# Kernel optimization log

Measured on AMD Instinct MI355X. Metric: run time of the kernel, lower is better.

The kernel has to match this reference:

```python
import jax, jax.numpy as jnp
import numpy as np

N = 51200      # num nodes
E = 614400     # num edges
G = 256        # num graphs
T = 8          # num target capsules (GCNConv heads)
D = 128        # in_channels == out_channels
ROUTES = 3     # num_routes
BN_EPS = 1e-5


def squash(s):
    # s: (..., D). v = |s|^2/(1+|s|^2) * s/|s|
    s2 = jnp.sum(s * s, axis=-1, keepdims=True)
    return (s2 / (1.0 + s2)) * s * jax.lax.rsqrt(s2 + 1e-16)


def setup_inputs() -> dict:
    key = jax.random.key(0)
    k0, k1, k2, k3 = jax.random.split(key, 4)
    x = jax.random.normal(k0, (N, D), dtype=jnp.float32)
    edge_index = jax.random.randint(k1, (2, E), 0, N, dtype=jnp.int32)
    batch = jnp.sort(jax.random.randint(k2, (N,), 0, G, dtype=jnp.int32))
    edge_weight = jnp.ones((E,), dtype=jnp.float32)
    gamma = jnp.ones((D,), dtype=jnp.float32)
    beta = jnp.zeros((D,), dtype=jnp.float32)
    W = jax.random.normal(k3, (T, D, D), dtype=jnp.float32) * (1.0 / np.sqrt(D))
    bias = jnp.zeros((T, D), dtype=jnp.float32)
    return {"x": x, "edge_weight": edge_weight, "gamma": gamma, "beta": beta,
            "W": W, "bias": bias, "edge_index": edge_index, "batch": batch}


def reference(x, edge_weight, gamma, beta, W, bias, edge_index, batch):
    n = x.shape[0]
    row, col = edge_index[0], edge_index[1]

    # BatchNorm1d (training-mode batch stats)
    mu = jnp.mean(x, axis=0)
    var = jnp.var(x, axis=0)
    x = (x - mu) * jax.lax.rsqrt(var + BN_EPS) * gamma + beta

    # --- GCNConv per target capsule (PyG gcn_norm with self-loops) ---
    sl = jnp.arange(n, dtype=row.dtype)
    row_sl = jnp.concatenate([row, sl])
    col_sl = jnp.concatenate([col, sl])
    w_sl = jnp.concatenate([edge_weight, jnp.ones((n,), x.dtype)])
    deg = jax.ops.segment_sum(w_sl, col_sl, num_segments=n)
    dis = jnp.where(deg > 0, jax.lax.rsqrt(jnp.maximum(deg, 1e-12)), 0.0)
    norm = dis[row_sl] * w_sl * dis[col_sl]          # (E+N,)

    xW = jnp.einsum('nd,tdo->nto', x, W)             # (N, T, D)
    caps = []
    for t in range(T):  # small fixed loop over capsule heads keeps edge msgs at (E+N, D)
        msg = norm[:, None] * xW[row_sl, t]          # (E+N, D)
        caps.append(jax.ops.segment_sum(msg, col_sl, num_segments=n) + bias[t])
    u_hat = jnp.stack(caps, axis=1)                  # (N, T, D)

    # --- dynamic routing ---
    node_deg = jax.ops.segment_sum(edge_weight, row, num_segments=n)  # original edges, no self loops
    b = jnp.broadcast_to(node_deg[:, None, None], (n, T, 1))
    u_det = jax.lax.stop_gradient(u_hat)
    for _ in range(ROUTES - 1):
        c = jax.nn.softmax(b, axis=1)                               # (N, T, 1)
        s = jax.ops.segment_sum(c * u_det, batch, num_segments=G)   # (G, T, D)
        v = squash(s)[batch]                                        # (N, T, D)
        b = b + jnp.sum(u_det * v, axis=-1, keepdims=True)

    c = jax.nn.softmax(b, axis=1)
    s = jax.ops.segment_sum(c * u_hat, batch, num_segments=G)        # (G, T, D)
    cnt = jax.ops.segment_sum(jnp.ones((n,), x.dtype), batch, num_segments=G)
    x_mean = jax.ops.segment_sum(x, batch, num_segments=G) / jnp.maximum(cnt, 1.0)[:, None]
    s = s + x_mean[:, None, :]
    v = squash(s)
    # final_layer=True: per-capsule L2 norm -> (G, T)
    return jnp.sqrt(jnp.sum(v * v, axis=-1) + 1e-16)
```

## Files before the change

### kernel.cpp

```cpp
#include <hip/hip_runtime.h>
#include <hip/hip_bf16.h>
#include <math.h>

#define N_NODES 51200
#define N_EDGES 614400
#define N_GRAPHS 256
#define T_CAPS 8
#define D_DIM 128
#define BN_EPS 1e-5f
#define RCAP 256
#define NBUCK 200
#define BCAP 4096
#define EPB 4096
#define SBLK 150
typedef __attribute__((ext_vector_type(8))) __bf16 bf16x8;
typedef __attribute__((ext_vector_type(8))) unsigned short ushort8;
typedef __attribute__((ext_vector_type(4))) float f32x4;

__device__ inline f32x4 mfma16(uint4 a, uint4 b, f32x4 c) {
  return __builtin_amdgcn_mfma_f32_16x16x32_bf16(
      __builtin_bit_cast(bf16x8, a), __builtin_bit_cast(bf16x8, b), c, 0, 0, 0);
}
__device__ inline f32x4 mfma16v(uint4 a, ushort8 b, f32x4 c) {
  return __builtin_amdgcn_mfma_f32_16x16x32_bf16(
      __builtin_bit_cast(bf16x8, a), __builtin_bit_cast(bf16x8, b), c, 0, 0, 0);
}

__device__ inline float waveReduceSum(float v) {
#pragma unroll
  for (int off = 1; off < 64; off <<= 1) v += __shfl_xor(v, off, 64);
  return v;
}
__device__ inline float bf_lo(unsigned u) { return __uint_as_float(u << 16); }
__device__ inline float bf_hi(unsigned u) { return __uint_as_float(u & 0xffff0000u); }
__device__ inline unsigned bfbits(float f) {
  unsigned u = __float_as_uint(f);
  return (u + 0x7FFFu + ((u >> 16) & 1u)) >> 16;
}

__global__ void __launch_bounds__(256) prep(const int* __restrict__ batch,
                                            const float* __restrict__ W,
                                            int* __restrict__ start, int* __restrict__ bcur,
                                            unsigned* __restrict__ Wfrag,
                                            unsigned* __restrict__ WTfrag,
                                            float* __restrict__ rawzero) {
  int i = blockIdx.x * 256 + threadIdx.x;
  if (i < NBUCK) bcur[i] = 0;
  for (int j = i; j < 2 * N_GRAPHS * D_DIM; j += N_NODES) rawzero[j] = 0.f;
  int bn = batch[i];
  if (i == 0) {
    for (int g = 0; g <= bn; g++) start[g] = 0;
  } else {
    int bp = batch[i - 1];
    for (int g = bp + 1; g <= bn; g++) start[g] = i;
  }
  if (i == N_NODES - 1)
    for (int g = bn + 1; g <= N_GRAPHS; g++) start[g] = N_NODES;
  for (int dd = i; dd < 65536; dd += N_NODES) {
    int jj = dd & 3, lane = (dd >> 2) & 63, ks = (dd >> 8) & 3;
    int nt = (dd >> 10) & 7, t = dd >> 13;
    int k = ks * 32 + ((lane >> 4) << 3) + 2 * jj;
    int n = nt * 16 + (lane & 15);
    float a = W[(t << 14) + (k << 7) + n];
    float b = W[(t << 14) + ((k + 1) << 7) + n];
    Wfrag[dd] = bfbits(a) | (bfbits(b) << 16);
    float2 w2 = ((const float2*)W)[((t << 14) + (n << 7) + k) >> 1];
    WTfrag[dd] = bfbits(w2.x) | (bfbits(w2.y) << 16);
  }
}

__global__ void __launch_bounds__(512) scatter_x(
    const int* __restrict__ row, const int* __restrict__ col, const float* __restrict__ ew,
    int* __restrict__ bcur, uint2* __restrict__ ebuck, const float* __restrict__ x,
    const int* __restrict__ start, float* __restrict__ rawxsum, float* __restrict__ rawxsq) {
  int bid = blockIdx.x, tid = threadIdx.x;
  __shared__ uint2 staged[EPB];
  __shared__ int hcnt[256], lbase[256], gbase[256], wpart[8];
  if (bid < SBLK) {
    unsigned rx[8], ry[8];
    int bk[8], idx[8];
    int e4 = bid * 1024 + tid;
#pragma unroll
    for (int h = 0; h < 2; h++) {
      int4 c4 = ((const int4*)col)[e4 + h * 512];
      int4 r4 = ((const int4*)row)[e4 + h * 512];
      float4 w4 = ((const float4*)ew)[e4 + h * 512];
      int o = h * 4;
      rx[o] = ((unsigned)c4.x << 16) | (unsigned)r4.x; ry[o] = bfbits(w4.x); bk[o] = c4.x >> 8;
      rx[o+1] = ((unsigned)c4.y << 16) | (unsigned)r4.y; ry[o+1] = bfbits(w4.y); bk[o+1] = c4.y >> 8;
      rx[o+2] = ((unsigned)c4.z << 16) | (unsigned)r4.z; ry[o+2] = bfbits(w4.z); bk[o+2] = c4.z >> 8;
      rx[o+3] = ((unsigned)c4.w << 16) | (unsigned)r4.w; ry[o+3] = bfbits(w4.w); bk[o+3] = c4.w >> 8;
    }
    if (tid < 256) hcnt[tid] = 0;
    __syncthreads();
#pragma unroll
    for (int k = 0; k < 8; k++) idx[k] = atomicAdd(&hcnt[bk[k]], 1);
    __syncthreads();
    int v = (tid < 256) ? hcnt[tid] : 0;
    int lane = tid & 63, wid = tid >> 6;
    int s = v;
#pragma unroll
    for (int off = 1; off < 64; off <<= 1) {
      int t = __shfl_up(s, off, 64);
      if (lane >= off) s += t;
    }
    if (lane == 63) wpart[wid] = s;
    if (tid < NBUCK) gbase[tid] = atomicAdd(&bcur[tid], v);
    __syncthreads();
    int add = 0;
    for (int w2 = 0; w2 < wid; w2++) add += wpart[w2];
    if (tid < 256) lbase[tid] = s + add - v;
    __syncthreads();
#pragma unroll
    for (int k = 0; k < 8; k++) staged[lbase[bk[k]] + idx[k]] = make_uint2(rx[k], ry[k]);
    __syncthreads();
    for (int i = tid; i < EPB; i += 512) {
      uint2 r = staged[i];
      int b = r.x >> 24;
      int pos = gbase[b] + (i - lbase[b]);
      if (pos < BCAP) ebuck[b * BCAP + pos] = r;
    }
    return;
  }
  int b2 = bid - SBLK;
  int g = b2 >> 2, sub = b2 & 3;
  float* ls = (float*)staged;
  float* ls2 = ls + 16 * 128;
  int q = tid & 31, h = tid >> 5;
  int st = start[g], en = start[g + 1];
  const float4* x4 = (const float4*)x;
  float4 s = make_float4(0.f, 0.f, 0.f, 0.f), s2 = make_float4(0.f, 0.f, 0.f, 0.f);
  for (int n = st + sub * 16 + h; n < en; n += 64) {
    float4 v = x4[n * 32 + q];
    s.x += v.x; s.y += v.y; s.z += v.z; s.w += v.w;
    s2.x += v.x * v.x; s2.y += v.y * v.y; s2.z += v.z * v.z; s2.w += v.w * v.w;
  }
  *(float4*)&ls[h * 128 + 4 * q] = s;
  *(float4*)&ls2[h * 128 + 4 * q] = s2;
  __syncthreads();
  if (tid < 128) {
    float a = 0.f;
#pragma unroll
    for (int hh = 0; hh < 16; hh++) a += ls[hh * 128 + tid];
    atomicAdd(&rawxsum[g * D_DIM + tid], a);
  } else if (tid < 256) {
    int d = tid - 128;
    float a = 0.f;
#pragma unroll
    for (int hh = 0; hh < 16; hh++) a += ls2[hh * 128 + d];
    atomicAdd(&rawxsq[g * D_DIM + d], a);
  }
}

__global__ void __launch_bounds__(512) mid(const float* __restrict__ rawxsum,
                                           const float* __restrict__ rawxsq,
                                           const float* __restrict__ gamma,
                                           const float* __restrict__ beta,
                                           float* __restrict__ scale,
                                           float* __restrict__ shift,
                                           const uint2* __restrict__ ebuck,
                                           const int* __restrict__ bcur,
                                           unsigned* __restrict__ csr,
                                           int* __restrict__ nstart, int* __restrict__ ncnt,
                                           float* __restrict__ dis) {
  int bid = blockIdx.x, tid = threadIdx.x;
  __shared__ uint2 staged[BCAP];
  __shared__ unsigned outr[BCAP];
  __shared__ int hist[256], pref[256], cur[256], wpart[8];
  if (bid < 128) {
    int d = bid;
    float* ls = (float*)staged;
    float* ls2 = ls + 256;
    if (tid < 256) {
      ls[tid] = rawxsum[tid * D_DIM + d];
      ls2[tid] = rawxsq[tid * D_DIM + d];
    }
    __syncthreads();
    for (int off = 128; off; off >>= 1) {
      if (tid < off) {
        ls[tid] += ls[tid + off];
        ls2[tid] += ls2[tid + off];
      }
      __syncthreads();
    }
    if (tid == 0) {
      float mu = ls[0] * (1.0f / N_NODES);
      float var = ls2[0] * (1.0f / N_NODES) - mu * mu;
      float rstd = rsqrtf(var + BN_EPS);
      float sc = gamma[d] * rstd;
      scale[d] = sc;
      shift[d] = beta[d] - mu * sc;
    }
    return;
  }
  int b = bid - 128;
  int cnt = min(bcur[b], BCAP);
  for (int i = tid; i < cnt; i += 512) staged[i] = ebuck[b * BCAP + i];
  if (tid < 256) hist[tid] = 0;
  __syncthreads();
  for (int i = tid; i < cnt; i += 512) {
    int dl = (staged[i].x >> 16) & 255;
    atomicAdd(&hist[dl], 1);
  }
  __syncthreads();
  int v = (tid < 256) ? hist[tid] : 0;
  int lane = tid & 63, wid = tid >> 6;
  int s = v;
#pragma unroll
  for (int off = 1; off < 64; off <<= 1) {
    int t = __shfl_up(s, off, 64);
    if (lane >= off) s += t;
  }
  if (lane == 63 && wid < 4) wpart[wid] = s;
  __syncthreads();
  int p0 = 0;
  if (tid < 256) {
    int add = 0;
    for (int w2 = 0; w2 < wid; w2++) add += wpart[w2];
    p0 = s + add - v;
    pref[tid] = p0;
    cur[tid] = p0;
  }
  __syncthreads();
  for (int i = tid; i < cnt; i += 512) {
    uint2 r = staged[i];
    int dl = (r.x >> 16) & 255;
    int p = atomicAdd(&cur[dl], 1);
    outr[p] = ((r.x & 0xFFFFu) << 16) | r.y;
  }
  __syncthreads();
  for (int i = tid; i < cnt; i += 512) csr[b * BCAP + i] = outr[i];
  if (tid < 256) {
    int n = b * 256 + tid;
    int hc = hist[tid];
    nstart[n] = b * BCAP + p0;
    ncnt[n] = hc;
    float sw = 0.f;
    for (int j = p0; j < p0 + hc; j++) sw += bf_lo(outr[j]);
    float dv = sw + 1.0f;
    dis[n] = dv > 0.f ? rsqrtf(fmaxf(dv, 1e-12f)) : 0.f;
  }
}

__global__ void __launch_bounds__(256) y_build(const float* __restrict__ x,
                                               const float* __restrict__ scale,
                                               const float* __restrict__ shift,
                                               const float* __restrict__ dis,
                                               __hip_bfloat162* __restrict__ y) {
  int base = blockIdx.x * 64;
  const float4* x4 = (const float4*)x;
  const float4* sc4 = (const float4*)scale;
  const float4* sh4 = (const float4*)shift;
  uint2* y2 = (uint2*)y;
  for (int i = threadIdx.x; i < 64 * 32; i += 256) {
    int nl = i >> 5, l = i & 31;
    int n = base + nl;
    float dnl = dis[n];
    float4 scv = sc4[l], shv = sh4[l];
    float4 xv = x4[n * 32 + l];
    unsigned u0 = bfbits(dnl * (xv.x * scv.x + shv.x)) |
                  (bfbits(dnl * (xv.y * scv.y + shv.y)) << 16);
    unsigned u1 = bfbits(dnl * (xv.z * scv.z + shv.z)) |
                  (bfbits(dnl * (xv.w * scv.w + shv.w)) << 16);
    y2[n * 32 + l] = make_uint2(u0, u1);
  }
}

__global__ void __launch_bounds__(256) node_gather(const __hip_bfloat162* __restrict__ y,
                                                   const float* __restrict__ dis,
                                                   const int* __restrict__ nstart,
                                                   const int* __restrict__ ncnt,
                                                   const unsigned* __restrict__ csr,
                                                   __hip_bfloat162* __restrict__ agg) {
  int n = blockIdx.x * 4 + (threadIdx.x >> 6);
  int lane = threadIdx.x & 63;
  int st = nstart[n], c = ncnt[n];
  float2 a = __bfloat1622float2(y[n * 64 + lane]);
  int j = 0;
  for (; j + 8 <= c; j += 8) {
    unsigned r[8];
#pragma unroll
    for (int k = 0; k < 8; k++) r[k] = csr[st + j + k];
    float2 v[8];
#pragma unroll
    for (int k = 0; k < 8; k++) v[k] = __bfloat1622float2(y[(r[k] >> 16) * 64 + lane]);
#pragma unroll
    for (int k = 0; k < 8; k++) {
      float w = bf_lo(r[k]);
      a.x += w * v[k].x;
      a.y += w * v[k].y;
    }
  }
  for (; j + 4 <= c; j += 4) {
    unsigned r0 = csr[st + j], r1 = csr[st + j + 1], r2 = csr[st + j + 2],
             r3 = csr[st + j + 3];
    float2 v0 = __bfloat1622float2(y[(r0 >> 16) * 64 + lane]);
    float2 v1 = __bfloat1622float2(y[(r1 >> 16) * 64 + lane]);
    float2 v2 = __bfloat1622float2(y[(r2 >> 16) * 64 + lane]);
    float2 v3 = __bfloat1622float2(y[(r3 >> 16) * 64 + lane]);
    float w0 = bf_lo(r0), w1 = bf_lo(r1), w2 = bf_lo(r2), w3 = bf_lo(r3);
    a.x += w0 * v0.x + w1 * v1.x + w2 * v2.x + w3 * v3.x;
    a.y += w0 * v0.y + w1 * v1.y + w2 * v2.y + w3 * v3.y;
  }
  for (; j < c; j++) {
    unsigned r = csr[st + j];
    float2 v = __bfloat1622float2(y[(r >> 16) * 64 + lane]);
    float w = bf_lo(r);
    a.x += w * v.x;
    a.y += w * v.y;
  }
  float dn = dis[n];
  a.x *= dn;
  a.y *= dn;
  agg[n * 64 + lane] = __float22bfloat162_rn(a);
}

__global__ void __launch_bounds__(1024, 4) routing_fused(
    const unsigned* __restrict__ agg_bf, const int* __restrict__ start,
    const unsigned* __restrict__ Wfrag, const unsigned* __restrict__ WTfrag,
    const float* __restrict__ bias, const float* __restrict__ rawxsum,
    const float* __restrict__ scale, const float* __restrict__ shift,
    float* __restrict__ out) {
  int g = blockIdx.x;
  int tid = threadIdx.x;
  int st = start[g], c = start[g + 1] - st;

  __shared__ unsigned ag_sh[RCAP * 68];
  __shared__ float dt_sh[384][T_CAPS];
  __shared__ float ac_sh[T_CAPS][D_DIM];
  __shared__ float s_sh[T_CAPS][D_DIM];
  __shared__ float wv_sh[T_CAPS][132];
  __shared__ unsigned wvpk[2][16][68];
  __shared__ unsigned short ctb[2][16][264];
  __shared__ unsigned acpk[T_CAPS][2][64];
  __shared__ unsigned spk[T_CAPS][2][64];
  __shared__ float csum_sh[T_CAPS], bv_sh[T_CAPS], f_sh[T_CAPS], s2p[T_CAPS][2];
  __shared__ float csp_sh[32];

  float* scratch = &dt_sh[0][0];
  const uint4* aggb4 = (const uint4*)agg_bf;
  uint4* ag4 = (uint4*)ag_sh;

  for (int i = tid; i < T_CAPS * 132; i += 1024) (&wv_sh[0][0])[i] = 0.f;
  for (int i = tid; i < 2 * 16 * 68; i += 1024) (&wvpk[0][0][0])[i] = 0u;
  for (int i = tid; i < 2 * 16 * 264; i += 1024) (&ctb[0][0][0])[i] = 0;
  if (tid < T_CAPS) {
    bv_sh[tid] = 0.f;
    csum_sh[tid] = 0.125f * (float)c;
  }
  {
    int d2 = tid & 63, h = tid >> 6;
    float sx = 0.f, sy = 0.f;
    for (int n = st + h; n < st + c; n += 16) {
      unsigned u = agg_bf[n * 64 + d2];
      sx += bf_lo(u);
      sy += bf_hi(u);
    }
    scratch[h * 128 + d2 * 2] = sx;
    scratch[h * 128 + d2 * 2 + 1] = sy;
  }
  __syncthreads();
  if (tid < 128) {
    float s = 0.f;
#pragma unroll
    for (int h = 0; h < 16; h++) s += scratch[h * 128 + tid];
    s *= 0.125f;
#pragma unroll
    for (int t = 0; t < T_CAPS; t++) ac_sh[t][tid] = s;
  }
  __syncthreads();

  int tG = tid >> 7, oG = tid & 127;
  int lane = tid & 63, wv_ = tid >> 6;

  for (int iter = 0; iter < 3; iter++) {
    {
      int t = tid >> 7, m = (tid >> 6) & 1, kp = tid & 63;
      float a = ac_sh[t][2 * kp], b = ac_sh[t][2 * kp + 1];
      unsigned ha = bfbits(a), hb = bfbits(b);
      if (m == 0)
        acpk[t][0][kp] = ha | (hb << 16);
      else
        acpk[t][1][kp] = bfbits(a - __uint_as_float(ha << 16)) |
                         (bfbits(b - __uint_as_float(hb << 16)) << 16);
    }
    __syncthreads();
    {
      int t = wv_ & 7, oh = wv_ >> 3;
      int m = lane & 15, q = lane >> 4;
      const uint4* Wf = (const uint4*)Wfrag;
#pragma unroll 1
      for (int cq = 0; cq < 4; cq++) {
        f32x4 C = {0.f, 0.f, 0.f, 0.f};
#pragma unroll
        for (int ks = 0; ks < 4; ks++) {
          uint4 A = (m < 2) ? *(const uint4*)&acpk[t][m][ks * 16 + q * 4]
                            : make_uint4(0, 0, 0, 0);
          uint4 B = Wf[((t * 8 + oh * 4 + cq) * 4 + ks) * 64 + lane];
          C = mfma16(A, B, C);
        }
        if (q == 0) s_sh[t][oh * 64 + cq * 16 + m] = C[0] + C[1];
      }
    }
    __syncthreads();
    {
      float s = s_sh[tG][oG] + csum_sh[tG] * bias[(tG << 7) + oG];
      if (iter == 2) {
        float cf = (float)c;
        float ic = 1.0f / fmaxf(cf, 1.0f);
        s += (scale[oG] * rawxsum[g * D_DIM + oG] + cf * shift[oG]) * ic;
      }
      s_sh[tG][oG] = s;
      float p = waveReduceSum(s * s);
      if ((tid & 63) == 0) s2p[tG][(tid >> 6) & 1] = p;
    }
    __syncthreads();
    {
      int t = tid >> 7, m = (tid >> 6) & 1, kp = tid & 63;
      float a = s_sh[t][2 * kp], b = s_sh[t][2 * kp + 1];
      unsigned ha = bfbits(a), hb = bfbits(b);
      if (m == 0)
        spk[t][0][kp] = ha | (hb << 16);
      else
        spk[t][1][kp] = bfbits(a - __uint_as_float(ha << 16)) |
                        (bfbits(b - __uint_as_float(hb << 16)) << 16);
    }
    if (tid < T_CAPS) {
      float s2 = s2p[tid][0] + s2p[tid][1];
      float f = (s2 / (1.0f + s2)) * rsqrtf(s2 + 1e-16f);
      f_sh[tid] = f;
      if (iter == 2) out[g * T_CAPS + tid] = sqrtf(f * f * s2 + 1e-16f);
    }
    __syncthreads();
    if (iter == 2) return;
    {
      int t = wv_ & 7, oh = wv_ >> 3;
      int m = lane & 15, q = lane >> 4;
      const uint4* Wf = (const uint4*)WTfrag;
#pragma unroll 1
      for (int cq = 0; cq < 4; cq++) {
        f32x4 C = {0.f, 0.f, 0.f, 0.f};
#pragma unroll
        for (int ks = 0; ks < 4; ks++) {
          uint4 A = (m < 2) ? *(const uint4*)&spk[t][m][ks * 16 + q * 4]
                            : make_uint4(0, 0, 0, 0);
          uint4 B = Wf[((t * 8 + oh * 4 + cq) * 4 + ks) * 64 + lane];
          C = mfma16(A, B, C);
        }
        if (q == 0) scratch[t * 128 + oh * 64 + cq * 16 + m] = C[0] + C[1];
      }
    }
    __syncthreads();
    {
      wv_sh[tG][oG] += f_sh[tG] * scratch[tG * 128 + oG];
      float bp = bias[(tG << 7) + oG] * s_sh[tG][oG];
      bp = waveReduceSum(bp);
      if ((tid & 63) == 0) s2p[tG][(tid >> 6) & 1] = bp;
    }
    __syncthreads();
    if (tid < T_CAPS) bv_sh[tid] += f_sh[tid] * (s2p[tid][0] + s2p[tid][1]);
    __syncthreads();
    for (int i = tid; i < 512; i += 1024) {
      int t = i >> 6, kp = i & 63;
      float a = wv_sh[t][2 * kp], b = wv_sh[t][2 * kp + 1];
      unsigned ha = bfbits(a), hb = bfbits(b);
      wvpk[0][t][kp] = ha | (hb << 16);
      float ra = a - __uint_as_float(ha << 16), rb = b - __uint_as_float(hb << 16);
      wvpk[1][t][kp] = bfbits(ra) | (bfbits(rb) << 16);
    }
    if (tid < 1024) {
      (&ac_sh[0][0])[tid] = 0.f;
    }
    if (tid < T_CAPS) csum_sh[tid] = 0.f;
    __syncthreads();

    for (int cb = 0; cb < c; cb += RCAP) {
      int nv = min(RCAP, c - cb);
      int KR32 = (nv + 31) & ~31;
      int Mt = (nv + 15) >> 4;
      if (iter == 0 || c > RCAP) {
        for (int i = tid; i < nv * 16; i += 1024) {
          int r = i >> 4, k = i & 15;
          ag4[r * 17 + k] = aggb4[(size_t)(st + cb + r) * 16 + k];
        }
        for (int i = tid; i < (KR32 - nv) * 16; i += 1024) {
          int r = nv + (i >> 4), k = i & 15;
          ag4[r * 17 + k] = make_uint4(0, 0, 0, 0);
        }
        __syncthreads();
      }
      if (wv_ < Mt) {
        int q = lane >> 4, tc = lane & 15;
        int r = wv_ * 16 + tc;
        const uint4* arow = ag4 + r * 17;
        f32x4 C = {0.f, 0.f, 0.f, 0.f};
#pragma unroll
        for (int ks = 0; ks < 4; ks++) {
          uint4 A = arow[ks * 4 + q];
          uint4 Bh = *(const uint4*)&wvpk[0][tc][ks * 16 + 4 * q];
          uint4 Bl = *(const uint4*)&wvpk[1][tc][ks * 16 + 4 * q];
          C = mfma16(A, Bh, C);
          C = mfma16(A, Bl, C);
        }
        if (tc < T_CAPS) {
          float bvv = bv_sh[tc];
#pragma unroll
          for (int i2 = 0; i2 < 4; i2++) dt_sh[wv_ * 16 + 4 * q + i2][tc] = C[i2] + bvv;
        }
      }
      __syncthreads();
      if (tid < nv) {
        float l[8];
#pragma unroll
        for (int t = 0; t < 8; t++) l[t] = dt_sh[tid][t];
        float m = l[0];
#pragma unroll
        for (int t = 1; t < 8; t++) m = fmaxf(m, l[t]);
        float z = 0.f;
#pragma unroll
        for (int t = 0; t < 8; t++) {
          l[t] = __expf(l[t] - m);
          z += l[t];
        }
        float iz = 1.0f / z;
#pragma unroll
        for (int t = 0; t < 8; t++) {
          float cv = l[t] * iz;
          dt_sh[tid][t] = cv;
          unsigned hb = bfbits(cv);
          ctb[0][t][tid] = (unsigned short)hb;
          ctb[1][t][tid] = (unsigned short)bfbits(cv - __uint_as_float(hb << 16));
        }
      }
      if (c > RCAP) {
        int tail = KR32 - nv;
        for (int i = tid; i < 16 * tail; i += 1024) {
          int hh = i & 1, t = (i >> 1) & 7, n2 = nv + (i >> 4);
          ctb[hh][t][n2] = 0;
        }
      }
      __syncthreads();
      {
        int tA = tid >> 7, idx = tid & 127;
        float p = 0.f;
        for (int n = idx; n < nv; n += 128) p += dt_sh[n][tA];
        p = waveReduceSum(p);
        if (lane == 0) csp_sh[wv_] = p;
      }
      __syncthreads();
      if (tid < T_CAPS) csum_sh[tid] += csp_sh[2 * tid] + csp_sh[2 * tid + 1];
      {
        int nt = wv_ & 7, kh = wv_ >> 3;
        int tc = lane & 15, q = lane >> 4;
        f32x4 C = {0.f, 0.f, 0.f, 0.f};
        const unsigned short* agh = (const unsigned short*)ag_sh;
        int KS = KR32 >> 5;
        for (int ks = kh; ks < KS; ks += 2) {
          uint4 Ah = *(const uint4*)&ctb[0][tc][ks * 32 + 8 * q];
          uint4 Al = *(const uint4*)&ctb[1][tc][ks * 32 + 8 * q];
          int nb = ks * 32 + 8 * q, dcol = nt * 16 + tc;
          ushort8 B;
#pragma unroll
          for (int j = 0; j < 8; j++) B[j] = agh[(nb + j) * 136 + dcol];
          C = mfma16v(Ah, B, C);
          C = mfma16v(Al, B, C);
        }
        if (kh == 1) *(f32x4*)&scratch[(nt * 64 + lane) * 4] = C;
        __syncthreads();
        if (kh == 0) {
          f32x4 o4 = *(const f32x4*)&scratch[(nt * 64 + lane) * 4];
          C.x += o4.x;
          C.y += o4.y;
          C.z += o4.z;
          C.w += o4.w;
#pragma unroll
          for (int i2 = 0; i2 < 4; i2++) {
            int tt = 4 * q + i2;
            if (tt < T_CAPS) ac_sh[tt][nt * 16 + tc] += C[i2];
          }
        }
      }
      __syncthreads();
    }
  }
}

extern "C" void kernel_launch(void* const* d_in, const int* in_sizes, int n_in, void* d_out,
                              int out_size, void* d_ws, size_t ws_size, hipStream_t stream) {
  const float* x = (const float*)d_in[0];
  const float* ew = (const float*)d_in[1];
  const float* gamma = (const float*)d_in[2];
  const float* beta = (const float*)d_in[3];
  const float* W = (const float*)d_in[4];
  const float* bias = (const float*)d_in[5];
  const int* eidx = (const int*)d_in[6];
  const int* batch = (const int*)d_in[7];
  float* out = (float*)d_out;
  float* w = (float*)d_ws;

  const int* row = eidx;
  const int* col = eidx + N_EDGES;

  int* bcur = (int*)w;
  int* start = bcur + 256;
  float* scale = (float*)(start + 260);
  float* shift = scale + 128;
  float* dis = shift + 128;
  float* rawxsum = dis + N_NODES;
  float* rawxsq = rawxsum + N_GRAPHS * D_DIM;
  unsigned* Wfrag = (unsigned*)(rawxsq + N_GRAPHS * D_DIM);
  unsigned* WTfrag = Wfrag + 65536;
  int* nstart = (int*)(WTfrag + 65536);
  int* ncnt = nstart + N_NODES;
  uint2* ebuck = (uint2*)(ncnt + N_NODES);
  unsigned* csr = (unsigned*)(ebuck + (size_t)NBUCK * BCAP);
  __hip_bfloat162* y = (__hip_bfloat162*)(csr + (size_t)NBUCK * BCAP);
  unsigned* agg_bf = (unsigned*)(y + (size_t)N_NODES * 64);

  prep<<<N_NODES / 256, 256, 0, stream>>>(batch, W, start, bcur, Wfrag, WTfrag, rawxsum);
  scatter_x<<<SBLK + 4 * N_GRAPHS, 512, 0, stream>>>(row, col, ew, bcur, ebuck, x, start,
                                                     rawxsum, rawxsq);
  mid<<<128 + NBUCK, 512, 0, stream>>>(rawxsum, rawxsq, gamma, beta, scale, shift, ebuck,
                                       bcur, csr, nstart, ncnt, dis);
  y_build<<<N_NODES / 64, 256, 0, stream>>>(x, scale, shift, dis, y);
  node_gather<<<N_NODES / 4, 256, 0, stream>>>(y, dis, nstart, ncnt, csr,
                                               (__hip_bfloat162*)agg_bf);
  routing_fused<<<N_GRAPHS, 1024, 0, stream>>>(agg_bf, start, Wfrag, WTfrag, bias, rawxsum,
                                               scale, shift, out);
}
```

Baseline: 173.1 us.

## Merge prep and scatter into one front kernel with partial-sum x stats

Folds the prep kernel (start offsets, W fragment packing) into the edge-scatter/x-statistics kernel as an extra block range, so one launch disappears. The x statistics blocks now find graph bounds by binary search over batch instead of depending on start, and write per-sub-block partial sums that mid reduces, replacing the global atomics and the zeroing pass. bcur is cleared with a memset instead. This trades a launch and atomics for a small extra buffer, a memset call and a redundant binary search per block.

Measured after the change: 180.0 us. 4.0% more time.

```diff
diff --git a/kernel.cpp b/kernel.cpp
--- a/kernel.cpp
+++ b/kernel.cpp
@@ -13,6 +13,8 @@
 #define BCAP 4096
 #define EPB 4096
 #define SBLK 150
+#define XBLK (4 * N_GRAPHS)
+#define PBLK 200
 typedef __attribute__((ext_vector_type(8))) __bf16 bf16x8;
 typedef __attribute__((ext_vector_type(8))) unsigned short ushort8;
 typedef __attribute__((ext_vector_type(4))) float f32x4;
@@ -38,25 +40,116 @@
   return (u + 0x7FFFu + ((u >> 16) & 1u)) >> 16;
 }
 
-__global__ void __launch_bounds__(256) prep(const int* __restrict__ batch,
-                                            const float* __restrict__ W,
-                                            int* __restrict__ start, int* __restrict__ bcur,
-                                            unsigned* __restrict__ Wfrag,
-                                            unsigned* __restrict__ WTfrag,
-                                            float* __restrict__ rawzero) {
-  int i = blockIdx.x * 256 + threadIdx.x;
-  if (i < NBUCK) bcur[i] = 0;
-  for (int j = i; j < 2 * N_GRAPHS * D_DIM; j += N_NODES) rawzero[j] = 0.f;
-  int bn = batch[i];
-  if (i == 0) {
-    for (int g = 0; g <= bn; g++) start[g] = 0;
-  } else {
-    int bp = batch[i - 1];
-    for (int g = bp + 1; g <= bn; g++) start[g] = i;
-  }
-  if (i == N_NODES - 1)
-    for (int g = bn + 1; g <= N_GRAPHS; g++) start[g] = N_NODES;
-  for (int dd = i; dd < 65536; dd += N_NODES) {
+__global__ void __launch_bounds__(512) front(
+    const int* __restrict__ row, const int* __restrict__ col, const float* __restrict__ ew,
+    int* __restrict__ bcur, uint2* __restrict__ ebuck, const float* __restrict__ x,
+    const int* __restrict__ batch, float* __restrict__ rawxp, float* __restrict__ rawxq,
+    int* __restrict__ start, const float* __restrict__ W, unsigned* __restrict__ Wfrag,
+    unsigned* __restrict__ WTfrag) {
+  int bid = blockIdx.x, tid = threadIdx.x;
+  if (bid < SBLK) {
+    __shared__ uint2 staged[EPB];
+    __shared__ int hcnt[256], lbase[256], gbase[256], wpart[8];
+    unsigned rx[8], ry[8];
+    int bk[8], idx[8];
+    int e4 = bid * 1024 + tid;
+#pragma unroll
+    for (int h = 0; h < 2; h++) {
+      int4 c4 = ((const int4*)col)[e4 + h * 512];
+      int4 r4 = ((const int4*)row)[e4 + h * 512];
+      float4 w4 = ((const float4*)ew)[e4 + h * 512];
+      int o = h * 4;
+      rx[o] = ((unsigned)c4.x << 16) | (unsigned)r4.x; ry[o] = bfbits(w4.x); bk[o] = c4.x >> 8;
+      rx[o+1] = ((unsigned)c4.y << 16) | (unsigned)r4.y; ry[o+1] = bfbits(w4.y); bk[o+1] = c4.y >> 8;
+      rx[o+2] = ((unsigned)c4.z << 16) | (unsigned)r4.z; ry[o+2] = bfbits(w4.z); bk[o+2] = c4.z >> 8;
+      rx[o+3] = ((unsigned)c4.w << 16) | (unsigned)r4.w; ry[o+3] = bfbits(w4.w); bk[o+3] = c4.w >> 8;
+    }
+    if (tid < 256) hcnt[tid] = 0;
+    __syncthreads();
+#pragma unroll
+    for (int k = 0; k < 8; k++) idx[k] = atomicAdd(&hcnt[bk[k]], 1);
+    __syncthreads();
+    int v = (tid < 256) ? hcnt[tid] : 0;
+    int lane = tid & 63, wid = tid >> 6;
+    int s = v;
+#pragma unroll
+    for (int off = 1; off < 64; off <<= 1) {
+      int t = __shfl_up(s, off, 64);
+      if (lane >= off) s += t;
+    }
+    if (lane == 63) wpart[wid] = s;
+    if (tid < NBUCK) gbase[tid] = atomicAdd(&bcur[tid], v);
+    __syncthreads();
+    int add = 0;
+    for (int w2 = 0; w2 < wid; w2++) add += wpart[w2];
+    if (tid < 256) lbase[tid] = s + add - v;
+    __syncthreads();
+#pragma unroll
+    for (int k = 0; k < 8; k++) staged[lbase[bk[k]] + idx[k]] = make_uint2(rx[k], ry[k]);
+    __syncthreads();
+    for (int i = tid; i < EPB; i += 512) {
+      uint2 r = staged[i];
+      int b = r.x >> 24;
+      int pos = gbase[b] + (i - lbase[b]);
+      if (pos < BCAP) ebuck[b * BCAP + pos] = r;
+    }
+    return;
+  }
+  if (bid < SBLK + XBLK) {
+    int b2 = bid - SBLK;
+    int g = b2 >> 2, sub = b2 & 3;
+    __shared__ float ls[16 * 128], ls2[16 * 128];
+    __shared__ int bounds[2];
+    if (tid < 2) {
+      int target = g + tid;
+      int lo = 0, hi = N_NODES;
+      while (lo < hi) {
+        int m = (lo + hi) >> 1;
+        if (batch[m] < target) lo = m + 1; else hi = m;
+      }
+      bounds[tid] = lo;
+    }
+    __syncthreads();
+    int st = bounds[0], en = bounds[1];
+    int q = tid & 31, h = tid >> 5;
+    const float4* x4 = (const float4*)x;
+    float4 s = make_float4(0.f, 0.f, 0.f, 0.f), s2 = make_float4(0.f, 0.f, 0.f, 0.f);
+    for (int n = st + sub * 16 + h; n < en; n += 64) {
+      float4 v = x4[n * 32 + q];
+      s.x += v.x; s.y += v.y; s.z += v.z; s.w += v.w;
+      s2.x += v.x * v.x; s2.y += v.y * v.y; s2.z += v.z * v.z; s2.w += v.w * v.w;
+    }
+    *(float4*)&ls[h * 128 + 4 * q] = s;
+    *(float4*)&ls2[h * 128 + 4 * q] = s2;
+    __syncthreads();
+    if (tid < 128) {
+      float a = 0.f;
+#pragma unroll
+      for (int hh = 0; hh < 16; hh++) a += ls[hh * 128 + tid];
+      rawxp[(sub * N_GRAPHS + g) * D_DIM + tid] = a;
+    } else if (tid < 256) {
+      int d = tid - 128;
+      float a = 0.f;
+#pragma unroll
+      for (int hh = 0; hh < 16; hh++) a += ls2[hh * 128 + d];
+      rawxq[(sub * N_GRAPHS + g) * D_DIM + d] = a;
+    }
+    return;
+  }
+  int pb = bid - SBLK - XBLK;
+  if (tid < 256) {
+    int i = pb * 256 + tid;
+    int bn = batch[i];
+    if (i == 0) {
+      for (int g = 0; g <= bn; g++) start[g] = 0;
+    } else {
+      int bp = batch[i - 1];
+      for (int g = bp + 1; g <= bn; g++) start[g] = i;
+    }
+    if (i == N_NODES - 1)
+      for (int g = bn + 1; g <= N_GRAPHS; g++) start[g] = N_NODES;
+  }
+  for (int dd = pb * 512 + tid; dd < 65536; dd += PBLK * 512) {
     int jj = dd & 3, lane = (dd >> 2) & 63, ks = (dd >> 8) & 3;
     int nt = (dd >> 10) & 7, t = dd >> 13;
     int k = ks * 32 + ((lane >> 4) << 3) + 2 * jj;
@@ -69,91 +162,9 @@
   }
 }
 
-__global__ void __launch_bounds__(512) scatter_x(
-    const int* __restrict__ row, const int* __restrict__ col, const float* __restrict__ ew,
-    int* __restrict__ bcur, uint2* __restrict__ ebuck, const float* __restrict__ x,
-    const int* __restrict__ start, float* __restrict__ rawxsum, float* __restrict__ rawxsq) {
-  int bid = blockIdx.x, tid = threadIdx.x;
-  __shared__ uint2 staged[EPB];
-  __shared__ int hcnt[256], lbase[256], gbase[256], wpart[8];
-  if (bid < SBLK) {
-    unsigned rx[8], ry[8];
-    int bk[8], idx[8];
-    int e4 = bid * 1024 + tid;
-#pragma unroll
-    for (int h = 0; h < 2; h++) {
-      int4 c4 = ((const int4*)col)[e4 + h * 512];
-      int4 r4 = ((const int4*)row)[e4 + h * 512];
-      float4 w4 = ((const float4*)ew)[e4 + h * 512];
-      int o = h * 4;
-      rx[o] = ((unsigned)c4.x << 16) | (unsigned)r4.x; ry[o] = bfbits(w4.x); bk[o] = c4.x >> 8;
-      rx[o+1] = ((unsigned)c4.y << 16) | (unsigned)r4.y; ry[o+1] = bfbits(w4.y); bk[o+1] = c4.y >> 8;
-      rx[o+2] = ((unsigned)c4.z << 16) | (unsigned)r4.z; ry[o+2] = bfbits(w4.z); bk[o+2] = c4.z >> 8;
-      rx[o+3] = ((unsigned)c4.w << 16) | (unsigned)r4.w; ry[o+3] = bfbits(w4.w); bk[o+3] = c4.w >> 8;
-    }
-    if (tid < 256) hcnt[tid] = 0;
-    __syncthreads();
-#pragma unroll
-    for (int k = 0; k < 8; k++) idx[k] = atomicAdd(&hcnt[bk[k]], 1);
-    __syncthreads();
-    int v = (tid < 256) ? hcnt[tid] : 0;
-    int lane = tid & 63, wid = tid >> 6;
-    int s = v;
-#pragma unroll
-    for (int off = 1; off < 64; off <<= 1) {
-      int t = __shfl_up(s, off, 64);
-      if (lane >= off) s += t;
-    }
-    if (lane == 63) wpart[wid] = s;
-    if (tid < NBUCK) gbase[tid] = atomicAdd(&bcur[tid], v);
-    __syncthreads();
-    int add = 0;
-    for (int w2 = 0; w2 < wid; w2++) add += wpart[w2];
-    if (tid < 256) lbase[tid] = s + add - v;
-    __syncthreads();
-#pragma unroll
-    for (int k = 0; k < 8; k++) staged[lbase[bk[k]] + idx[k]] = make_uint2(rx[k], ry[k]);
-    __syncthreads();
-    for (int i = tid; i < EPB; i += 512) {
-      uint2 r = staged[i];
-      int b = r.x >> 24;
-      int pos = gbase[b] + (i - lbase[b]);
-      if (pos < BCAP) ebuck[b * BCAP + pos] = r;
-    }
-    return;
-  }
-  int b2 = bid - SBLK;
-  int g = b2 >> 2, sub = b2 & 3;
-  float* ls = (float*)staged;
-  float* ls2 = ls + 16 * 128;
-  int q = tid & 31, h = tid >> 5;
-  int st = start[g], en = start[g + 1];
-  const float4* x4 = (const float4*)x;
-  float4 s = make_float4(0.f, 0.f, 0.f, 0.f), s2 = make_float4(0.f, 0.f, 0.f, 0.f);
-  for (int n = st + sub * 16 + h; n < en; n += 64) {
-    float4 v = x4[n * 32 + q];
-    s.x += v.x; s.y += v.y; s.z += v.z; s.w += v.w;
-    s2.x += v.x * v.x; s2.y += v.y * v.y; s2.z += v.z * v.z; s2.w += v.w * v.w;
-  }
-  *(float4*)&ls[h * 128 + 4 * q] = s;
-  *(float4*)&ls2[h * 128 + 4 * q] = s2;
-  __syncthreads();
-  if (tid < 128) {
-    float a = 0.f;
-#pragma unroll
-    for (int hh = 0; hh < 16; hh++) a += ls[hh * 128 + tid];
-    atomicAdd(&rawxsum[g * D_DIM + tid], a);
-  } else if (tid < 256) {
-    int d = tid - 128;
-    float a = 0.f;
-#pragma unroll
-    for (int hh = 0; hh < 16; hh++) a += ls2[hh * 128 + d];
-    atomicAdd(&rawxsq[g * D_DIM + d], a);
-  }
-}
-
-__global__ void __launch_bounds__(512) mid(const float* __restrict__ rawxsum,
-                                           const float* __restrict__ rawxsq,
+__global__ void __launch_bounds__(512) mid(const float* __restrict__ rawxp,
+                                           const float* __restrict__ rawxq,
+                                           float* __restrict__ rawxsum,
                                            const float* __restrict__ gamma,
                                            const float* __restrict__ beta,
                                            float* __restrict__ scale,
@@ -172,8 +183,15 @@
     float* ls = (float*)staged;
     float* ls2 = ls + 256;
     if (tid < 256) {
-      ls[tid] = rawxsum[tid * D_DIM + d];
-      ls2[tid] = rawxsq[tid * D_DIM + d];
+      float a = 0.f, a2 = 0.f;
+#pragma unroll
+      for (int s5 = 0; s5 < 4; s5++) {
+        a += rawxp[(s5 * N_GRAPHS + tid) * D_DIM + d];
+        a2 += rawxq[(s5 * N_GRAPHS + tid) * D_DIM + d];
+      }
+      rawxsum[tid * D_DIM + d] = a;
+      ls[tid] = a;
+      ls2[tid] = a2;
     }
     __syncthreads();
     for (int off = 128; off; off >>= 1) {
@@ -607,8 +625,9 @@
   float* shift = scale + 128;
   float* dis = shift + 128;
   float* rawxsum = dis + N_NODES;
-  float* rawxsq = rawxsum + N_GRAPHS * D_DIM;
-  unsigned* Wfrag = (unsigned*)(rawxsq + N_GRAPHS * D_DIM);
+  float* rawxp = rawxsum + N_GRAPHS * D_DIM;
+  float* rawxq = rawxp + 4 * N_GRAPHS * D_DIM;
+  unsigned* Wfrag = (unsigned*)(rawxq + 4 * N_GRAPHS * D_DIM);
   unsigned* WTfrag = Wfrag + 65536;
   int* nstart = (int*)(WTfrag + 65536);
   int* ncnt = nstart + N_NODES;
@@ -617,11 +636,11 @@
   __hip_bfloat162* y = (__hip_bfloat162*)(csr + (size_t)NBUCK * BCAP);
   unsigned* agg_bf = (unsigned*)(y + (size_t)N_NODES * 64);
 
-  prep<<<N_NODES / 256, 256, 0, stream>>>(batch, W, start, bcur, Wfrag, WTfrag, rawxsum);
-  scatter_x<<<SBLK + 4 * N_GRAPHS, 512, 0, stream>>>(row, col, ew, bcur, ebuck, x, start,
-                                                     rawxsum, rawxsq);
-  mid<<<128 + NBUCK, 512, 0, stream>>>(rawxsum, rawxsq, gamma, beta, scale, shift, ebuck,
-                                       bcur, csr, nstart, ncnt, dis);
+  hipMemsetAsync(bcur, 0, 256 * sizeof(int), stream);
+  front<<<SBLK + XBLK + PBLK, 512, 0, stream>>>(row, col, ew, bcur, ebuck, x, batch, rawxp,
+                                                rawxq, start, W, Wfrag, WTfrag);
+  mid<<<128 + NBUCK, 512, 0, stream>>>(rawxp, rawxq, rawxsum, gamma, beta, scale, shift,
+                                       ebuck, bcur, csr, nstart, ncnt, dis);
   y_build<<<N_NODES / 64, 256, 0, stream>>>(x, scale, shift, dis, y);
   node_gather<<<N_NODES / 4, 256, 0, stream>>>(y, dis, nstart, ncnt, csr,
                                                (__hip_bfloat162*)agg_bf);
```
